# Performance work log

Measured on AMD Instinct MI355X. Metric: run time of the kernel, lower is better.

Reference implementation:

```python
import jax, jax.numpy as jnp
import numpy as np

HEADS = 4
WS = 4
EPS = 1e-5

def _pw(x, w, b):
    # 1x1 conv: w is (out_c, in_c)
    return jnp.einsum('oc,bchw->bohw', w, x) + b[None, :, None, None]

def _dw(x, w, b, stride):
    # depthwise 5x5 conv, padding 2; w is (C,1,5,5) OIHW with groups=C
    c = x.shape[1]
    y = jax.lax.conv_general_dilated(x, w, (stride, stride), [(2, 2), (2, 2)],
                                     feature_group_count=c,
                                     dimension_numbers=('NCHW', 'OIHW', 'NCHW'))
    return y + b[None, :, None, None]

def _bn(x, g, bt, m, v):
    # inference-mode batchnorm
    return (x - m[None, :, None, None]) * (g / jnp.sqrt(v + EPS))[None, :, None, None] + bt[None, :, None, None]

def _fasa(x, q_w, q_b, kv_w, kv_b, local_w, local_b, mixer_w, mixer_b,
          p0_w, p0_b, bn0_g, bn0_b, bn0_m, bn0_v, lin0_w, lin0_b,
          p1_w, p1_b, bn1_g, bn1_b, bn1_m, bn1_v):
    b, c, h, w = x.shape
    H, W = h // WS, w // WS
    dh = c // HEADS
    q_local = _pw(x, q_w, q_b)
    # refined_downsample pool: dwconv(s2)+bn+1x1, dwconv(s2)+bn
    p = _dw(x, p0_w, p0_b, 2)
    p = _bn(p, bn0_g, bn0_b, bn0_m, bn0_v)
    p = _pw(p, lin0_w, lin0_b)
    p = _dw(p, p1_w, p1_b, 2)
    p = _bn(p, bn1_g, bn1_b, bn1_m, bn1_v)
    kv = _pw(p, kv_w, kv_b)                               # (b, 2c, H, W)
    q = q_local.reshape(b, HEADS, dh, h * w).transpose(0, 1, 3, 2)   # (b,h,hw,dh)
    kv = kv.reshape(b, 2, HEADS, dh, H * W).transpose(1, 0, 2, 4, 3) # (2,b,h,HW,dh)
    k, v = kv[0], kv[1]
    scale = dh ** -0.5
    attn = jax.nn.softmax(scale * jnp.einsum('bhqd,bhkd->bhqk', q, k), axis=-1)
    gf = jnp.einsum('bhqk,bhkd->bhqd', attn, v)           # (b,h,hw,dh)
    gf = gf.transpose(0, 1, 3, 2).reshape(b, c, h, w)
    lf = _dw(q_local, local_w, local_b, 1)
    lf = lf * jax.nn.sigmoid(lf)        # local_feat * local_weight
    lf = lf * jax.nn.sigmoid(gf)        # local_feat * local2global
    return _pw(lf * gf, mixer_w, mixer_b)

def setup_inputs() -> dict:
    key = jax.random.key(0)
    ks = jax.random.split(key, 24)
    B, C, Hh, Ww, K = 4, 128, 128, 128, 5
    s = 0.05
    d = {
        'x': jax.random.normal(ks[0], (B, C, Hh, Ww), jnp.float32),
        'q_w': jax.random.normal(ks[1], (C, C), jnp.float32) * s,
        'q_b': jnp.zeros((C,), jnp.float32),
        'kv_w': jax.random.normal(ks[2], (2 * C, C), jnp.float32) * s,
        'kv_b': jnp.zeros((2 * C,), jnp.float32),
        'local_w': jax.random.normal(ks[3], (C, 1, K, K), jnp.float32) * s,
        'local_b': jnp.zeros((C,), jnp.float32),
        'mixer_w': jax.random.normal(ks[4], (C, C), jnp.float32) * s,
        'mixer_b': jnp.zeros((C,), jnp.float32),
        'p0_w': jax.random.normal(ks[5], (C, 1, K, K), jnp.float32) * s,
        'p0_b': jnp.zeros((C,), jnp.float32),
        'bn0_g': jnp.ones((C,), jnp.float32),
        'bn0_b': jnp.zeros((C,), jnp.float32),
        'bn0_m': jax.random.normal(ks[6], (C,), jnp.float32) * 0.1,
        'bn0_v': jax.random.uniform(ks[7], (C,), jnp.float32) + 0.5,
        'lin0_w': jax.random.normal(ks[8], (C, C), jnp.float32) * s,
        'lin0_b': jnp.zeros((C,), jnp.float32),
        'p1_w': jax.random.normal(ks[9], (C, 1, K, K), jnp.float32) * s,
        'p1_b': jnp.zeros((C,), jnp.float32),
        'bn1_g': jnp.ones((C,), jnp.float32),
        'bn1_b': jnp.zeros((C,), jnp.float32),
        'bn1_m': jax.random.normal(ks[10], (C,), jnp.float32) * 0.1,
        'bn1_v': jax.random.uniform(ks[11], (C,), jnp.float32) + 0.5,
    }
    return d

def reference(x, q_w, q_b, kv_w, kv_b, local_w, local_b, mixer_w, mixer_b,
              p0_w, p0_b, bn0_g, bn0_b, bn0_m, bn0_v, lin0_w, lin0_b,
              p1_w, p1_b, bn1_g, bn1_b, bn1_m, bn1_v):
    return _fasa(x, q_w, q_b, kv_w, kv_b, local_w, local_b, mixer_w, mixer_b,
                 p0_w, p0_b, bn0_g, bn0_b, bn0_m, bn0_v, lin0_w, lin0_b,
                 p1_w, p1_b, bn1_g, bn1_b, bn1_m, bn1_v)
```

## Files before the change

### kernel.cpp

```cpp
#include <hip/hip_runtime.h>
#include <hip/hip_bf16.h>
#include <math.h>


#define NB   4
#define NC   128
#define NH   128
#define NW   128
#define NHW  16384
#define NKV  1024

typedef float    f32x4  __attribute__((ext_vector_type(4)));
typedef float    f32x16 __attribute__((ext_vector_type(16)));
typedef short    bf16x8 __attribute__((ext_vector_type(8)));
typedef unsigned u32x4v __attribute__((ext_vector_type(4)));

__device__ __forceinline__ unsigned short f2bf(float f) {
  unsigned u = __float_as_uint(f);
  u += 0x7FFF + ((u >> 16) & 1);
  return (unsigned short)(u >> 16);
}

__device__ __forceinline__ float bf2f(unsigned short u) {
  return __uint_as_float((unsigned)u << 16);
}

__device__ __forceinline__ unsigned cvtpk(float lo, float hi) {
  unsigned r;
  asm("v_cvt_pk_bf16_f32 %0, %1, %2" : "=v"(r) : "v"(lo), "v"(hi));
  return r;
}

template<bool IN_BF16, bool OUT_BF16>
__global__ __launch_bounds__(256) void pw_gemm_mfma(
    const float* __restrict__ Wmat,
    const float* __restrict__ bias,
    const void* __restrict__ Xv,
    void* __restrict__ Yv,
    int npos, int Mtot)
{
  __shared__ short Wlds[128 * 136];

  const int t  = threadIdx.x;
  const int w    = t >> 6;
  const int lane = t & 63;
  const int nl   = lane & 31;
  const int hi   = lane >> 5;
  const int b  = blockIdx.z;
  const int m0 = blockIdx.y * 128;
  const int n0 = blockIdx.x * 128;

  for (int i = t; i < 128 * 32; i += 256) {
    int row = i >> 5, c4 = (i & 31) * 4;
    float4 wv = *(const float4*)&Wmat[(size_t)(m0 + row) * 128 + c4];
    uint2 pk; pk.x = cvtpk(wv.x, wv.y); pk.y = cvtpk(wv.z, wv.w);
    *(uint2*)&Wlds[row * 136 + c4] = pk;
  }
  __syncthreads();

  f32x16 acc[4];
  #pragma unroll
  for (int mg = 0; mg < 4; mg++)
    #pragma unroll
    for (int r = 0; r < 16; r++) acc[mg][r] = 0.f;

  #pragma unroll
  for (int s = 0; s < 8; s++) {
    bf16x8 bfrag;
    if constexpr (IN_BF16) {
      const unsigned short* Xb = (const unsigned short*)Xv
          + (size_t)b * 128 * npos + n0 + w * 32 + nl;
      const unsigned short* xp = Xb + (size_t)(s * 16 + hi * 8) * npos;
      #pragma unroll
      for (int e = 0; e < 8; e++) bfrag[e] = (short)xp[(size_t)e * npos];
    } else {
      const float* Xb = (const float*)Xv + (size_t)b * 128 * npos + n0 + w * 32 + nl;
      const float* xp = Xb + (size_t)(s * 16 + hi * 8) * npos;
      float xv[8];
      #pragma unroll
      for (int e = 0; e < 8; e++) xv[e] = xp[(size_t)e * npos];
      u32x4v bu;
      #pragma unroll
      for (int j = 0; j < 4; j++) bu[j] = cvtpk(xv[2 * j], xv[2 * j + 1]);
      bfrag = __builtin_bit_cast(bf16x8, bu);
    }

    #pragma unroll
    for (int mg = 0; mg < 4; mg++) {
      bf16x8 afrag = *(const bf16x8*)&Wlds[(mg * 32 + nl) * 136 + s * 16 + hi * 8];
      acc[mg] = __builtin_amdgcn_mfma_f32_32x32x16_bf16(afrag, bfrag, acc[mg], 0, 0, 0);
    }
  }

  #pragma unroll
  for (int mg = 0; mg < 4; mg++)
    #pragma unroll
    for (int r = 0; r < 16; r++) {
      int drow = mg * 32 + (r & 3) + 8 * (r >> 2) + 4 * hi;
      float val = acc[mg][r] + bias[m0 + drow];
      if constexpr (OUT_BF16) {
        unsigned short* Yb = (unsigned short*)Yv
            + ((size_t)b * Mtot + m0) * npos + n0 + w * 32 + nl;
        Yb[(size_t)drow * npos] = f2bf(val);
      } else {
        float* Yb = (float*)Yv + ((size_t)b * Mtot + m0) * npos + n0 + w * 32 + nl;
        Yb[(size_t)drow * npos] = val;
      }
    }
}

template<int INH, int INW, int OUTW, int ORPB, int WLSP>
__global__ __launch_bounds__(256) void dw5x5s2_tile(
    const float* __restrict__ in,
    const float* __restrict__ wt, const float* __restrict__ bias,
    const float* __restrict__ g, const float* __restrict__ bt,
    const float* __restrict__ mean, const float* __restrict__ var,
    float* __restrict__ out)
{
  constexpr int IR = 2 * ORPB + 3;
  constexpr int XG = OUTW / 4;
  __shared__ float Ls[IR * WLSP];

  const int t  = threadIdx.x;
  const int c  = blockIdx.y, b = blockIdx.z;
  const int y0 = blockIdx.x * ORPB;
  const float* plane = in + ((size_t)b * NC + c) * INH * INW;

  for (int i = t; i < IR * WLSP / 4; i += 256)
    *(float4*)&Ls[i * 4] = (float4){0.f, 0.f, 0.f, 0.f};
  __syncthreads();

  for (int i = t; i < IR * (INW / 4); i += 256) {
    int r = i / (INW / 4), s4 = (i % (INW / 4)) * 4;
    int gy = 2 * y0 - 2 + r;
    if (gy >= 0 && gy < INH)
      *(float4*)&Ls[r * WLSP + 4 + s4] = *(const float4*)&plane[(size_t)gy * INW + s4];
  }

  float wreg[25];
  #pragma unroll
  for (int i = 0; i < 25; i++) wreg[i] = wt[c * 25 + i];
  const float sc = g[c] * rsqrtf(var[c] + 1e-5f);
  const float off = (bias[c] - mean[c]) * sc + bt[c];
  __syncthreads();

  const int row = t / XG;
  const int x0  = (t % XG) * 4;
  const int r0  = 2 * row;

  float a[4] = {0.f, 0.f, 0.f, 0.f};
  #pragma unroll
  for (int i = 0; i < 5; i++) {
    const float* lr = &Ls[(r0 + i) * WLSP + 2 * x0];
    float4 L0 = *(const float4*)&lr[0];
    float4 L1 = *(const float4*)&lr[4];
    float4 L2 = *(const float4*)&lr[8];
    float4 L3 = *(const float4*)&lr[12];
    float rr[16] = {L0.x,L0.y,L0.z,L0.w, L1.x,L1.y,L1.z,L1.w,
                    L2.x,L2.y,L2.z,L2.w, L3.x,L3.y,L3.z,L3.w};
    #pragma unroll
    for (int j = 0; j < 5; j++) {
      float wv = wreg[i * 5 + j];
      #pragma unroll
      for (int o = 0; o < 4; o++)
        a[o] += wv * rr[2 * o + j + 2];
    }
  }

  float4 ov;
  ov.x = a[0] * sc + off; ov.y = a[1] * sc + off;
  ov.z = a[2] * sc + off; ov.w = a[3] * sc + off;
  const int OH = INH / 2;
  *(float4*)&out[((size_t)b * NC + c) * OH * OUTW + (size_t)(y0 + row) * OUTW + x0] = ov;
}

__global__ __launch_bounds__(256) void kv_prep(
    const float* __restrict__ kvb,
    short* __restrict__ kT, short* __restrict__ vT)
{
  const int t = threadIdx.x;
  const int h = blockIdx.y, b = blockIdx.z;
  const int kpos = blockIdx.x * 256 + t;
  const int bh = b * 4 + h;

  bf16x8 kr[4];
  #pragma unroll
  for (int d = 0; d < 32; d++) {
    float kvv = kvb[((size_t)b * 256 + h * 32 + d) * NKV + kpos];
    float vvv = kvb[((size_t)b * 256 + 128 + h * 32 + d) * NKV + kpos];
    kr[d >> 3][d & 7] = (short)f2bf(kvv);
    vT[(size_t)bh * 32768 + d * NKV + kpos] = (short)f2bf(vvv);
  }
  short* dstk = kT + (size_t)bh * 32768 + (size_t)kpos * 32;
  #pragma unroll
  for (int i = 0; i < 4; i++)
    *(bf16x8*)(dstk + i * 8) = kr[i];
}

__global__ __launch_bounds__(512) void attn_mfma64(
    const unsigned short* __restrict__ q16,
    const short* __restrict__ kT,
    const short* __restrict__ vT,
    float* __restrict__ gf)
{
  __shared__ float Cmb[4][64][34];

  const int t    = threadIdx.x;
  const int w    = t >> 6;
  const int lane = t & 63;
  const int c    = lane & 31;
  const int hi   = lane >> 5;
  const int qg   = w & 3;
  const int half = w >> 2;
  const int b    = blockIdx.z, h = blockIdx.y;
  const int q0   = blockIdx.x * 256 + qg * 64;
  const int bh   = b * 4 + h;
  const int base = half * 16;

  const float QSCALE = 0.17677669529663689f * 1.4426950408889634f;

  bf16x8 qA1, qA2, qB1, qB2;
  {
    const unsigned short* qb = q16 + ((size_t)(b * NC + h * 32 + hi * 8)) * NHW + q0 + c;
    float fva[16], fvb[16];
    #pragma unroll
    for (int e = 0; e < 8; e++) {
      fva[e]     = bf2f(qb[(size_t)e * NHW]) * QSCALE;
      fva[8 + e] = bf2f(qb[(size_t)(16 + e) * NHW]) * QSCALE;
      fvb[e]     = bf2f(qb[(size_t)e * NHW + 32]) * QSCALE;
      fvb[8 + e] = bf2f(qb[(size_t)(16 + e) * NHW + 32]) * QSCALE;
    }
    u32x4v u1, u2, u3, u4;
    #pragma unroll
    for (int j = 0; j < 4; j++) {
      u1[j] = cvtpk(fva[2 * j], fva[2 * j + 1]);
      u2[j] = cvtpk(fva[8 + 2 * j], fva[9 + 2 * j]);
      u3[j] = cvtpk(fvb[2 * j], fvb[2 * j + 1]);
      u4[j] = cvtpk(fvb[8 + 2 * j], fvb[9 + 2 * j]);
    }
    qA1 = __builtin_bit_cast(bf16x8, u1); qA2 = __builtin_bit_cast(bf16x8, u2);
    qB1 = __builtin_bit_cast(bf16x8, u3); qB2 = __builtin_bit_cast(bf16x8, u4);
  }

  const short* kbh = kT + (size_t)bh * 32768;
  const short* vbh = vT + (size_t)bh * 32768;

  f32x16 oA, oB;
  #pragma unroll
  for (int r = 0; r < 16; r++) { oA[r] = 0.f; oB[r] = 0.f; }
  const f32x16 zf = oA;
  float lsumA = 0.f, lsumB = 0.f;

  const int kbase = base * 32;
  bf16x8 ka  = *(const bf16x8*)(kbh + (size_t)(kbase + c) * 32 + hi * 8);
  bf16x8 kb2 = *(const bf16x8*)(kbh + (size_t)(kbase + c) * 32 + 16 + hi * 8);
  bf16x8 va  = *(const bf16x8*)(vbh + (size_t)c * NKV + kbase + hi * 8);
  bf16x8 vb2 = *(const bf16x8*)(vbh + (size_t)c * NKV + kbase + 16 + hi * 8);

  for (int kt = 0; kt < 16; kt++) {
    const int k0n = (kt < 15) ? (kbase + (kt + 1) * 32) : 0;
    bf16x8 nka  = *(const bf16x8*)(kbh + (size_t)(k0n + c) * 32 + hi * 8);
    bf16x8 nkb  = *(const bf16x8*)(kbh + (size_t)(k0n + c) * 32 + 16 + hi * 8);
    bf16x8 nva  = *(const bf16x8*)(vbh + (size_t)c * NKV + k0n + hi * 8);
    bf16x8 nvb  = *(const bf16x8*)(vbh + (size_t)c * NKV + k0n + 16 + hi * 8);

    {
      f32x16 s = __builtin_amdgcn_mfma_f32_32x32x16_bf16(ka,  qA1, zf, 0, 0, 0);
      s        = __builtin_amdgcn_mfma_f32_32x32x16_bf16(kb2, qA2, s,  0, 0, 0);
      float p[16];
      #pragma unroll
      for (int r = 0; r < 16; r++) p[r] = __builtin_amdgcn_exp2f(s[r]);
      float s0 = (p[0] + p[1]) + (p[2] + p[3]);
      float s1 = (p[4] + p[5]) + (p[6] + p[7]);
      float s2 = (p[8] + p[9]) + (p[10] + p[11]);
      float s3 = (p[12] + p[13]) + (p[14] + p[15]);
      lsumA += (s0 + s1) + (s2 + s3);

      unsigned a0 = cvtpk(p[0],  p[1]);
      unsigned a1 = cvtpk(p[2],  p[3]);
      unsigned a2 = cvtpk(p[4],  p[5]);
      unsigned a3 = cvtpk(p[6],  p[7]);
      unsigned a4 = cvtpk(p[8],  p[9]);
      unsigned a5 = cvtpk(p[10], p[11]);
      unsigned a6 = cvtpk(p[12], p[13]);
      unsigned a7 = cvtpk(p[14], p[15]);
      asm("v_permlane32_swap_b32 %0, %1" : "+v"(a0), "+v"(a2));
      asm("v_permlane32_swap_b32 %0, %1" : "+v"(a1), "+v"(a3));
      asm("v_permlane32_swap_b32 %0, %1" : "+v"(a4), "+v"(a6));
      asm("v_permlane32_swap_b32 %0, %1" : "+v"(a5), "+v"(a7));
      u32x4v b1u = {a0, a1, a2, a3};
      u32x4v b2u = {a4, a5, a6, a7};
      bf16x8 pb1 = __builtin_bit_cast(bf16x8, b1u);
      bf16x8 pb2 = __builtin_bit_cast(bf16x8, b2u);
      oA = __builtin_amdgcn_mfma_f32_32x32x16_bf16(va,  pb1, oA, 0, 0, 0);
      oA = __builtin_amdgcn_mfma_f32_32x32x16_bf16(vb2, pb2, oA, 0, 0, 0);
    }

    {
      f32x16 s = __builtin_amdgcn_mfma_f32_32x32x16_bf16(ka,  qB1, zf, 0, 0, 0);
      s        = __builtin_amdgcn_mfma_f32_32x32x16_bf16(kb2, qB2, s,  0, 0, 0);
      float p[16];
      #pragma unroll
      for (int r = 0; r < 16; r++) p[r] = __builtin_amdgcn_exp2f(s[r]);
      float s0 = (p[0] + p[1]) + (p[2] + p[3]);
      float s1 = (p[4] + p[5]) + (p[6] + p[7]);
      float s2 = (p[8] + p[9]) + (p[10] + p[11]);
      float s3 = (p[12] + p[13]) + (p[14] + p[15]);
      lsumB += (s0 + s1) + (s2 + s3);

      unsigned a0 = cvtpk(p[0],  p[1]);
      unsigned a1 = cvtpk(p[2],  p[3]);
      unsigned a2 = cvtpk(p[4],  p[5]);
      unsigned a3 = cvtpk(p[6],  p[7]);
      unsigned a4 = cvtpk(p[8],  p[9]);
      unsigned a5 = cvtpk(p[10], p[11]);
      unsigned a6 = cvtpk(p[12], p[13]);
      unsigned a7 = cvtpk(p[14], p[15]);
      asm("v_permlane32_swap_b32 %0, %1" : "+v"(a0), "+v"(a2));
      asm("v_permlane32_swap_b32 %0, %1" : "+v"(a1), "+v"(a3));
      asm("v_permlane32_swap_b32 %0, %1" : "+v"(a4), "+v"(a6));
      asm("v_permlane32_swap_b32 %0, %1" : "+v"(a5), "+v"(a7));
      u32x4v b1u = {a0, a1, a2, a3};
      u32x4v b2u = {a4, a5, a6, a7};
      bf16x8 pb1 = __builtin_bit_cast(bf16x8, b1u);
      bf16x8 pb2 = __builtin_bit_cast(bf16x8, b2u);
      oB = __builtin_amdgcn_mfma_f32_32x32x16_bf16(va,  pb1, oB, 0, 0, 0);
      oB = __builtin_amdgcn_mfma_f32_32x32x16_bf16(vb2, pb2, oB, 0, 0, 0);
    }

    ka = nka; kb2 = nkb; va = nva; vb2 = nvb;
  }

  if (half) {
    float* dst = &Cmb[qg][lane][0];
    #pragma unroll
    for (int r = 0; r < 16; r++) { dst[r] = oA[r]; dst[16 + r] = oB[r]; }
    dst[32] = lsumA; dst[33] = lsumB;
  }
  __syncthreads();
  if (!half) {
    const float* src = &Cmb[qg][lane][0];
    #pragma unroll
    for (int r = 0; r < 16; r++) { oA[r] += src[r]; oB[r] += src[16 + r]; }
    lsumA += src[32]; lsumB += src[33];

    lsumA += __shfl_xor(lsumA, 32);
    lsumB += __shfl_xor(lsumB, 32);
    float invA = 1.f / lsumA;
    float invB = 1.f / lsumB;

    float* gfb = gf + ((size_t)(b * NC + h * 32)) * NHW + q0 + c;
    #pragma unroll
    for (int r = 0; r < 16; r++) {
      int d = (r & 3) + 8 * (r >> 2) + 4 * hi;
      gfb[(size_t)d * NHW]      = oA[r] * invA;
      gfb[(size_t)d * NHW + 32] = oB[r] * invB;
    }
  }
}

__global__ __launch_bounds__(256) void lf_fuse_tile(
    const unsigned short* __restrict__ q16, const float* __restrict__ gf,
    const float* __restrict__ wt, const float* __restrict__ bias,
    unsigned short* __restrict__ t16)
{
  __shared__ float Ls[12 * 140];

  const int t  = threadIdx.x;
  const int c  = blockIdx.y, b = blockIdx.z;
  const int y0 = blockIdx.x * 8;
  const unsigned short* plane = q16 + ((size_t)b * NC + c) * NHW;

  for (int i = t; i < 12 * 140 / 4; i += 256)
    *(float4*)&Ls[i * 4] = (float4){0.f, 0.f, 0.f, 0.f};
  __syncthreads();

  for (int i = t; i < 12 * 16; i += 256) {
    int r = i >> 4, s8 = (i & 15) * 8;
    int gy = y0 - 2 + r;
    if (gy >= 0 && gy < NH) {
      bf16x8 v = *(const bf16x8*)&plane[(size_t)gy * NW + s8];
      float* dp = &Ls[r * 140 + 4 + s8];
      #pragma unroll
      for (int j = 0; j < 8; j++) dp[j] = bf2f((unsigned short)v[j]);
    }
  }

  float wreg[25];
  #pragma unroll
  for (int i = 0; i < 25; i++) wreg[i] = wt[c * 25 + i];
  const float bs = bias[c];
  __syncthreads();

  const int row = t >> 5;
  const int x0  = (t & 31) * 4;

  float a[4] = {bs, bs, bs, bs};
  #pragma unroll
  for (int i = 0; i < 5; i++) {
    const float* lr = &Ls[(row + i) * 140 + x0];
    float4 L0 = *(const float4*)&lr[0];
    float4 L1 = *(const float4*)&lr[4];
    float4 L2 = *(const float4*)&lr[8];
    float rr[12] = {L0.x,L0.y,L0.z,L0.w, L1.x,L1.y,L1.z,L1.w,
                    L2.x,L2.y,L2.z,L2.w};
    #pragma unroll
    for (int j = 0; j < 5; j++) {
      float wv = wreg[i * 5 + j];
      #pragma unroll
      for (int o = 0; o < 4; o++)
        a[o] += wv * rr[o + j + 2];
    }
  }

  size_t base = ((size_t)b * NC + c) * NHW + (size_t)(y0 + row) * NW + x0;
  float4 gv4 = *(const float4*)&gf[base];
  float gvv[4] = {gv4.x, gv4.y, gv4.z, gv4.w};
  float op[4];
  #pragma unroll
  for (int k = 0; k < 4; k++) {
    float sl = a[k] / (1.f + __expf(-a[k]));
    float sg = 1.f / (1.f + __expf(-gvv[k]));
    op[k] = sl * sg * gvv[k];
  }
  uint2 ov;
  ov.x = cvtpk(op[0], op[1]);
  ov.y = cvtpk(op[2], op[3]);
  *(uint2*)&t16[base] = ov;
}

extern "C" void kernel_launch(void* const* d_in, const int* in_sizes, int n_in,
                              void* d_out, int out_size, void* d_ws, size_t ws_size,
                              hipStream_t stream) {
  const float* x       = (const float*)d_in[0];
  const float* q_w     = (const float*)d_in[1];
  const float* q_b     = (const float*)d_in[2];
  const float* kv_w    = (const float*)d_in[3];
  const float* kv_b    = (const float*)d_in[4];
  const float* local_w = (const float*)d_in[5];
  const float* local_b = (const float*)d_in[6];
  const float* mixer_w = (const float*)d_in[7];
  const float* mixer_b = (const float*)d_in[8];
  const float* p0_w    = (const float*)d_in[9];
  const float* p0_b    = (const float*)d_in[10];
  const float* bn0_g   = (const float*)d_in[11];
  const float* bn0_b   = (const float*)d_in[12];
  const float* bn0_m   = (const float*)d_in[13];
  const float* bn0_v   = (const float*)d_in[14];
  const float* lin0_w  = (const float*)d_in[15];
  const float* lin0_b  = (const float*)d_in[16];
  const float* p1_w    = (const float*)d_in[17];
  const float* p1_b    = (const float*)d_in[18];
  const float* bn1_g   = (const float*)d_in[19];
  const float* bn1_b   = (const float*)d_in[20];
  const float* bn1_m   = (const float*)d_in[21];
  const float* bn1_v   = (const float*)d_in[22];

  float* ws = (float*)d_ws;
  unsigned short* q16 = (unsigned short*)ws;
  float* gf   = ws + 4194304;
  unsigned short* t16 = (unsigned short*)(ws + 12582912);
  float* p0   = ws + 16777216;
  float* lin0b= ws + 18874368;
  float* p1   = ws + 20971520;
  float* kvb  = ws + 21495808;
  short* kT   = (short*)(ws + 22544384);
  short* vT   = kT + 524288;

  pw_gemm_mfma<false, true><<<dim3(NHW / 128, 1, NB), 256, 0, stream>>>(
      q_w, q_b, x, q16, NHW, 128);
  dw5x5s2_tile<128, 128, 64, 16, 140><<<dim3(4, NC, NB), 256, 0, stream>>>(
      x, p0_w, p0_b, bn0_g, bn0_b, bn0_m, bn0_v, p0);
  pw_gemm_mfma<false, false><<<dim3(4096 / 128, 1, NB), 256, 0, stream>>>(
      lin0_w, lin0_b, p0, lin0b, 4096, 128);
  dw5x5s2_tile<64, 64, 32, 32, 76><<<dim3(1, NC, NB), 256, 0, stream>>>(
      lin0b, p1_w, p1_b, bn1_g, bn1_b, bn1_m, bn1_v, p1);
  pw_gemm_mfma<false, false><<<dim3(NKV / 128, 2, NB), 256, 0, stream>>>(
      kv_w, kv_b, p1, kvb, NKV, 256);
  kv_prep<<<dim3(4, 4, NB), 256, 0, stream>>>(kvb, kT, vT);
  attn_mfma64<<<dim3(NHW / 256, 4, NB), 512, 0, stream>>>(q16, kT, vT, gf);
  lf_fuse_tile<<<dim3(16, NC, NB), 256, 0, stream>>>(q16, gf, local_w, local_b, t16);
  pw_gemm_mfma<true, false><<<dim3(NHW / 128, 1, NB), 256, 0, stream>>>(
      mixer_w, mixer_b, t16, (float*)d_out, NHW, 128);
}
```

Measured before the change: 153.4 us.

## Pre-convert weights to bf16, store attention output in bf16, shrink attention blocks

Adds a small kernel that converts all four pointwise weight matrices to bf16 once, so each GEMM block reads its A fragments straight from global memory instead of staging and converting them in LDS. The attention output gf is now written and read as bf16 rather than fp32, halving that intermediate's traffic into the fused local kernel. The attention kernel goes from 512-thread blocks covering 256 queries to 256-thread blocks covering 128 queries, with the two key halves combined through a smaller LDS buffer. The costs are an extra launch, uncoalesced global weight reads in the GEMM, and some extra rounding error in gf.

After: 169.0 us. 1.1x slower.

```diff
diff --git a/kernel.cpp b/kernel.cpp
--- a/kernel.cpp
+++ b/kernel.cpp
@@ -13,6 +13,7 @@
 typedef float    f32x4  __attribute__((ext_vector_type(4)));
 typedef float    f32x16 __attribute__((ext_vector_type(16)));
 typedef short    bf16x8 __attribute__((ext_vector_type(8)));
+typedef short    bf16x4 __attribute__((ext_vector_type(4)));
 typedef unsigned u32x4v __attribute__((ext_vector_type(4)));
 
 __device__ __forceinline__ unsigned short f2bf(float f) {
@@ -31,16 +32,29 @@
   return r;
 }
 
+__global__ __launch_bounds__(256) void wcvt(
+    const float* __restrict__ a, const float* __restrict__ bsrc,
+    const float* __restrict__ csrc, const float* __restrict__ dsrc,
+    unsigned short* __restrict__ o)
+{
+  int base = (blockIdx.x * 256 + threadIdx.x) * 4;
+  float4 v;
+  if (base < 16384)        v = *(const float4*)&a[base];
+  else if (base < 32768)   v = *(const float4*)&bsrc[base - 16384];
+  else if (base < 65536)   v = *(const float4*)&csrc[base - 32768];
+  else                     v = *(const float4*)&dsrc[base - 65536];
+  uint2 pk; pk.x = cvtpk(v.x, v.y); pk.y = cvtpk(v.z, v.w);
+  *(uint2*)&o[base] = pk;
+}
+
 template<bool IN_BF16, bool OUT_BF16>
 __global__ __launch_bounds__(256) void pw_gemm_mfma(
-    const float* __restrict__ Wmat,
+    const unsigned short* __restrict__ Wbf,
     const float* __restrict__ bias,
     const void* __restrict__ Xv,
     void* __restrict__ Yv,
     int npos, int Mtot)
 {
-  __shared__ short Wlds[128 * 136];
-
   const int t  = threadIdx.x;
   const int w    = t >> 6;
   const int lane = t & 63;
@@ -50,14 +64,6 @@
   const int m0 = blockIdx.y * 128;
   const int n0 = blockIdx.x * 128;
 
-  for (int i = t; i < 128 * 32; i += 256) {
-    int row = i >> 5, c4 = (i & 31) * 4;
-    float4 wv = *(const float4*)&Wmat[(size_t)(m0 + row) * 128 + c4];
-    uint2 pk; pk.x = cvtpk(wv.x, wv.y); pk.y = cvtpk(wv.z, wv.w);
-    *(uint2*)&Wlds[row * 136 + c4] = pk;
-  }
-  __syncthreads();
-
   f32x16 acc[4];
   #pragma unroll
   for (int mg = 0; mg < 4; mg++)
@@ -87,7 +93,7 @@
 
     #pragma unroll
     for (int mg = 0; mg < 4; mg++) {
-      bf16x8 afrag = *(const bf16x8*)&Wlds[(mg * 32 + nl) * 136 + s * 16 + hi * 8];
+      bf16x8 afrag = *(const bf16x8*)&Wbf[(size_t)(m0 + mg * 32 + nl) * 128 + s * 16 + hi * 8];
       acc[mg] = __builtin_amdgcn_mfma_f32_32x32x16_bf16(afrag, bfrag, acc[mg], 0, 0, 0);
     }
   }
@@ -197,25 +203,25 @@
     *(bf16x8*)(dstk + i * 8) = kr[i];
 }
 
-__global__ __launch_bounds__(512) void attn_mfma64(
+__global__ __launch_bounds__(256) void attn_mfma64(
     const unsigned short* __restrict__ q16,
     const short* __restrict__ kT,
     const short* __restrict__ vT,
-    float* __restrict__ gf)
-{
-  __shared__ float Cmb[4][64][34];
+    unsigned short* __restrict__ gf16)
+{
+  __shared__ float Cmb[2][64][34];
 
   const int t    = threadIdx.x;
   const int w    = t >> 6;
   const int lane = t & 63;
   const int c    = lane & 31;
   const int hi   = lane >> 5;
-  const int qg   = w & 3;
-  const int half = w >> 2;
+  const int qg   = w & 1;
+  const int half = w >> 1;
   const int b    = blockIdx.z, h = blockIdx.y;
-  const int q0   = blockIdx.x * 256 + qg * 64;
+  const int q0   = blockIdx.x * 128 + qg * 64;
   const int bh   = b * 4 + h;
-  const int base = half * 16;
+  const int kbase = half * 512;
 
   const float QSCALE = 0.17677669529663689f * 1.4426950408889634f;
 
@@ -251,7 +257,6 @@
   const f32x16 zf = oA;
   float lsumA = 0.f, lsumB = 0.f;
 
-  const int kbase = base * 32;
   bf16x8 ka  = *(const bf16x8*)(kbh + (size_t)(kbase + c) * 32 + hi * 8);
   bf16x8 kb2 = *(const bf16x8*)(kbh + (size_t)(kbase + c) * 32 + 16 + hi * 8);
   bf16x8 va  = *(const bf16x8*)(vbh + (size_t)c * NKV + kbase + hi * 8);
@@ -349,18 +354,18 @@
     float invA = 1.f / lsumA;
     float invB = 1.f / lsumB;
 
-    float* gfb = gf + ((size_t)(b * NC + h * 32)) * NHW + q0 + c;
+    unsigned short* gfb = gf16 + ((size_t)(b * NC + h * 32)) * NHW + q0 + c;
     #pragma unroll
     for (int r = 0; r < 16; r++) {
       int d = (r & 3) + 8 * (r >> 2) + 4 * hi;
-      gfb[(size_t)d * NHW]      = oA[r] * invA;
-      gfb[(size_t)d * NHW + 32] = oB[r] * invB;
+      gfb[(size_t)d * NHW]      = f2bf(oA[r] * invA);
+      gfb[(size_t)d * NHW + 32] = f2bf(oB[r] * invB);
     }
   }
 }
 
 __global__ __launch_bounds__(256) void lf_fuse_tile(
-    const unsigned short* __restrict__ q16, const float* __restrict__ gf,
+    const unsigned short* __restrict__ q16, const unsigned short* __restrict__ gf16,
     const float* __restrict__ wt, const float* __restrict__ bias,
     unsigned short* __restrict__ t16)
 {
@@ -414,14 +419,14 @@
   }
 
   size_t base = ((size_t)b * NC + c) * NHW + (size_t)(y0 + row) * NW + x0;
-  float4 gv4 = *(const float4*)&gf[base];
-  float gvv[4] = {gv4.x, gv4.y, gv4.z, gv4.w};
+  bf16x4 gv = *(const bf16x4*)&gf16[base];
   float op[4];
   #pragma unroll
   for (int k = 0; k < 4; k++) {
+    float gvv = bf2f((unsigned short)gv[k]);
     float sl = a[k] / (1.f + __expf(-a[k]));
-    float sg = 1.f / (1.f + __expf(-gvv[k]));
-    op[k] = sl * sg * gvv[k];
+    float sg = 1.f / (1.f + __expf(-gvv));
+    op[k] = sl * sg * gvv;
   }
   uint2 ov;
   ov.x = cvtpk(op[0], op[1]);
@@ -458,28 +463,30 @@
 
   float* ws = (float*)d_ws;
   unsigned short* q16 = (unsigned short*)ws;
-  float* gf   = ws + 4194304;
-  unsigned short* t16 = (unsigned short*)(ws + 12582912);
-  float* p0   = ws + 16777216;
-  float* lin0b= ws + 18874368;
-  float* p1   = ws + 20971520;
-  float* kvb  = ws + 21495808;
-  short* kT   = (short*)(ws + 22544384);
+  unsigned short* gf16 = (unsigned short*)(ws + 4194304);
+  unsigned short* t16 = (unsigned short*)(ws + 8388608);
+  float* p0   = ws + 12582912;
+  float* lin0b= ws + 14680064;
+  float* p1   = ws + 16777216;
+  float* kvb  = ws + 17301504;
+  short* kT   = (short*)(ws + 18350080);
   short* vT   = kT + 524288;
-
+  unsigned short* wbf = (unsigned short*)(ws + 18874368);
+
+  wcvt<<<dim3(80), 256, 0, stream>>>(q_w, lin0_w, kv_w, mixer_w, wbf);
   pw_gemm_mfma<false, true><<<dim3(NHW / 128, 1, NB), 256, 0, stream>>>(
-      q_w, q_b, x, q16, NHW, 128);
+      wbf, q_b, x, q16, NHW, 128);
   dw5x5s2_tile<128, 128, 64, 16, 140><<<dim3(4, NC, NB), 256, 0, stream>>>(
       x, p0_w, p0_b, bn0_g, bn0_b, bn0_m, bn0_v, p0);
   pw_gemm_mfma<false, false><<<dim3(4096 / 128, 1, NB), 256, 0, stream>>>(
-      lin0_w, lin0_b, p0, lin0b, 4096, 128);
+      wbf + 16384, lin0_b, p0, lin0b, 4096, 128);
   dw5x5s2_tile<64, 64, 32, 32, 76><<<dim3(1, NC, NB), 256, 0, stream>>>(
       lin0b, p1_w, p1_b, bn1_g, bn1_b, bn1_m, bn1_v, p1);
   pw_gemm_mfma<false, false><<<dim3(NKV / 128, 2, NB), 256, 0, stream>>>(
-      kv_w, kv_b, p1, kvb, NKV, 256);
+      wbf + 32768, kv_b, p1, kvb, NKV, 256);
   kv_prep<<<dim3(4, 4, NB), 256, 0, stream>>>(kvb, kT, vT);
-  attn_mfma64<<<dim3(NHW / 256, 4, NB), 512, 0, stream>>>(q16, kT, vT, gf);
-  lf_fuse_tile<<<dim3(16, NC, NB), 256, 0, stream>>>(q16, gf, local_w, local_b, t16);
+  attn_mfma64<<<dim3(NHW / 128, 4, NB), 256, 0, stream>>>(q16, kT, vT, gf16);
+  lf_fuse_tile<<<dim3(16, NC, NB), 256, 0, stream>>>(q16, gf16, local_w, local_b, t16);
   pw_gemm_mfma<true, false><<<dim3(NHW / 128, 1, NB), 256, 0, stream>>>(
-      mixer_w, mixer_b, t16, (float*)d_out, NHW, 128);
-}
+      wbf + 65536, mixer_b, t16, (float*)d_out, NHW, 128);
+}
```
